# Performance work log

Hardware: AMD Instinct MI355X
Metric: run time of the kernel (lower is better)

The kernel has to match this reference:

```python
import jax, jax.numpy as jnp
import numpy as np

B, K, N = 8, 4, 131072
T = B * K * N  # upper bound on packed length
NEG_IDLE = -1e8   # logit value forced when slot is idle
NEG_FILL = -1000.0  # padded-output fill value for logits


def setup_inputs() -> dict:
    key = jax.random.key(0)
    k1, k2, k3, k4, k5, k6 = jax.random.split(key, 6)
    return {
        "rgb": jax.random.normal(k1, (T, 3), dtype=jnp.float32),
        "logits_surface": jax.random.normal(k2, (T, 1), dtype=jnp.float32),
        "logits_air": jax.random.normal(k3, (T, 1), dtype=jnp.float32),
        "mask_surface": jax.random.bernoulli(k4, 0.5, (B, K, N)),
        "mask_air": jax.random.bernoulli(k5, 0.5, (B, K, N)),
        "idle_states": jax.random.uniform(k6, (B, K), dtype=jnp.float32),
    }


def reference(rgb, logits_surface, logits_air, mask_surface, mask_air, idle_states):
    # Packed arrays are laid out in flattened (b, k, n) order: the packed index of a
    # masked element equals the count of True entries preceding it -> cumsum - 1.
    Bb, Kk, Nn = mask_surface.shape
    scale = (1.0 - idle_states)[:, :, None, None]          # [B,K,1,1]
    idle = idle_states[:, :, None, None]                   # [B,K,1,1]

    ms_flat = mask_surface.reshape(-1)
    idx_s = (jnp.cumsum(ms_flat.astype(jnp.int32)) - 1).reshape(Bb, Kk, Nn)
    ms = mask_surface[..., None]                           # [B,K,N,1]

    rgb_g = jnp.take(rgb, idx_s, axis=0)                   # [B,K,N,3]
    rgb_out = jnp.where(ms, rgb_g * scale, 0.0)

    ls_g = jnp.take(logits_surface, idx_s, axis=0)         # [B,K,N,1]
    logits_surface_out = jnp.where(ms, ls_g * scale + idle * NEG_IDLE, NEG_FILL)

    ma_flat = mask_air.reshape(-1)
    idx_a = (jnp.cumsum(ma_flat.astype(jnp.int32)) - 1).reshape(Bb, Kk, Nn)
    ma = mask_air[..., None]
    la_g = jnp.take(logits_air, idx_a, axis=0)             # [B,K,N,1]
    logits_air_out = jnp.where(ma, la_g * scale + idle * NEG_IDLE, NEG_FILL)

    return rgb_out, logits_surface_out, logits_air_out
```

## Files before the change

kernel.cpp:

```cpp
#include <hip/hip_runtime.h>
#include <stdint.h>

#define T_TOTAL  4194304
#define NEG_IDLE (-100000000.0f)
#define NEG_FILL (-1000.0f)

#define BLOCK   256
#define EPT     8
#define EPB     (BLOCK * EPT)
#define NBLOCKS (T_TOTAL / EPB)


typedef unsigned int u32x4 __attribute__((ext_vector_type(4)));

__device__ __forceinline__ unsigned decode8_i32(const u32x4 a, const u32x4 b) {
    return (a.x ? 1u : 0u) | (a.y ? 2u : 0u) | (a.z ? 4u : 0u) | (a.w ? 8u : 0u)
         | (b.x ? 16u : 0u) | (b.y ? 32u : 0u) | (b.z ? 64u : 0u) | (b.w ? 128u : 0u);
}

__global__ __launch_bounds__(BLOCK) void reduce_pack_kernel(
    const u32x4* __restrict__ ms,
    const u32x4* __restrict__ ma,
    unsigned long long* __restrict__ sums,
    unsigned short* __restrict__ packed)
{
    const int blk  = blockIdx.x;
    const int tid  = threadIdx.x;
    const int lane = tid & 63;
    const int wave = tid >> 6;
    const size_t e = (size_t)blk * EPB + (size_t)tid * EPT;

    const u32x4* ps = ms + (e >> 2);
    const u32x4* pa = ma + (e >> 2);
    const u32x4 s0 = __builtin_nontemporal_load(ps);
    const u32x4 s1 = __builtin_nontemporal_load(ps + 1);
    const u32x4 a0 = __builtin_nontemporal_load(pa);
    const u32x4 a1 = __builtin_nontemporal_load(pa + 1);
    const unsigned bits_s = decode8_i32(s0, s1);
    const unsigned bits_a = decode8_i32(a0, a1);
    packed[blk * BLOCK + tid] = (unsigned short)(bits_s | (bits_a << 8));

    unsigned long long v =
        ((unsigned long long)(unsigned)__popc(bits_a) << 32) | (unsigned)__popc(bits_s);
    #pragma unroll
    for (int d = 32; d; d >>= 1) v += __shfl_down(v, d, 64);

    __shared__ unsigned long long w[BLOCK / 64];
    if (lane == 0) w[wave] = v;
    __syncthreads();
    if (tid == 0) sums[blk] = w[0] + w[1] + w[2] + w[3];
}

__global__ __launch_bounds__(BLOCK) void scatter_kernel(
    const float* __restrict__ rgb,
    const float* __restrict__ ls,
    const float* __restrict__ la,
    const unsigned long long* __restrict__ sums,
    const unsigned short* __restrict__ packed,
    const float* __restrict__ idle_states,
    float* __restrict__ out)
{
    const int blk  = blockIdx.x;
    const int tid  = threadIdx.x;
    const int lane = tid & 63;
    const int wave = tid >> 6;
    const size_t base = (size_t)blk * EPB + (size_t)tid * EPT;

    const unsigned p = packed[blk * BLOCK + tid];
    const unsigned bits_s = p & 0xffu;
    const unsigned bits_a = p >> 8;

    unsigned long long acc = 0;
    {
        const ulonglong2* s2 = (const ulonglong2*)sums;
        const int i0 = lane * 32;
        #pragma unroll
        for (int q = 0; q < 16; ++q) {
            const ulonglong2 v = s2[lane * 16 + q];
            const int i = i0 + 2 * q;
            acc += (i     < blk) ? v.x : 0ull;
            acc += (i + 1 < blk) ? v.y : 0ull;
        }
    }
    #pragma unroll
    for (int w = 0; w < BLOCK / 64 - 1; ++w) {
        if (w < wave) {
            const unsigned pp = packed[blk * BLOCK + w * 64 + lane];
            acc += ((unsigned long long)(unsigned)__popc(pp >> 8) << 32)
                 | (unsigned)__popc(pp & 0xffu);
        }
    }
    #pragma unroll
    for (int d = 32; d; d >>= 1) acc += __shfl_xor(acc, d, 64);

    const unsigned long long pk =
        ((unsigned long long)(unsigned)__popc(bits_a) << 32) | (unsigned)__popc(bits_s);
    unsigned long long incl = pk;
    #pragma unroll
    for (int d = 1; d < 64; d <<= 1) {
        unsigned long long t = __shfl_up(incl, d, 64);
        if (lane >= d) incl += t;
    }
    const unsigned long long start = acc + (incl - pk);

    const int idx_s0 = (int)(start & 0xffffffffULL);
    const int idx_a0 = (int)(start >> 32);

    int is_[EPT], ia_[EPT];
    #pragma unroll
    for (int j = 0; j < EPT; ++j) {
        is_[j] = idx_s0 + __popc(bits_s & ((1u << j) - 1u));
        ia_[j] = idx_a0 + __popc(bits_a & ((1u << j) - 1u));
    }

    float r[3 * EPT], sv[EPT], av[EPT];
    #pragma unroll
    for (int j = 0; j < EPT; ++j) {
        const float* rp = rgb + (size_t)is_[j] * 3;
        r[3 * j + 0] = rp[0];
        r[3 * j + 1] = rp[1];
        r[3 * j + 2] = rp[2];
        sv[j] = ls[is_[j]];
        av[j] = la[ia_[j]];
    }

    const float idle      = idle_states[blk >> 6];
    const float scale     = 1.0f - idle;
    const float idle_term = idle * NEG_IDLE;
    #pragma unroll
    for (int j = 0; j < EPT; ++j) {
        const bool bs = (bits_s >> j) & 1u;
        const bool ba = (bits_a >> j) & 1u;
        r[3 * j + 0] = bs ? r[3 * j + 0] * scale : 0.0f;
        r[3 * j + 1] = bs ? r[3 * j + 1] * scale : 0.0f;
        r[3 * j + 2] = bs ? r[3 * j + 2] * scale : 0.0f;
        sv[j] = bs ? (sv[j] * scale + idle_term) : NEG_FILL;
        av[j] = ba ? (av[j] * scale + idle_term) : NEG_FILL;
    }

    float4* prgb = (float4*)(out + base * 3);
    #pragma unroll
    for (int j = 0; j < 6; ++j) prgb[j] = ((const float4*)r)[j];

    float4* pls = (float4*)(out + (size_t)3 * T_TOTAL + base);
    pls[0] = ((const float4*)sv)[0];
    pls[1] = ((const float4*)sv)[1];

    float4* pla = (float4*)(out + (size_t)4 * T_TOTAL + base);
    pla[0] = ((const float4*)av)[0];
    pla[1] = ((const float4*)av)[1];
}

extern "C" void kernel_launch(void* const* d_in, const int* in_sizes, int n_in,
                              void* d_out, int out_size, void* d_ws, size_t ws_size,
                              hipStream_t stream) {
    const float* rgb  = (const float*)d_in[0];
    const float* ls   = (const float*)d_in[1];
    const float* la   = (const float*)d_in[2];
    const u32x4* ms   = (const u32x4*)d_in[3];
    const u32x4* ma   = (const u32x4*)d_in[4];
    const float* idle = (const float*)d_in[5];
    float* out = (float*)d_out;

    unsigned long long* sums   = (unsigned long long*)d_ws;
    unsigned short*     packed = (unsigned short*)((uint8_t*)d_ws + NBLOCKS * sizeof(unsigned long long));

    reduce_pack_kernel<<<NBLOCKS, BLOCK, 0, stream>>>(ms, ma, sums, packed);
    scatter_kernel<<<NBLOCKS, BLOCK, 0, stream>>>(rgb, ls, la, sums, packed,
                                                  idle, out);
}
```

Measured before the change: 204.4 us.

## Stage surface gathers through LDS with coalesced block loads and swizzled stores

Each block now loads its contiguous range of packed rgb and surface logits into shared memory with coalesced loads, then gathers from LDS instead of doing scattered global loads. The rgb output is transposed through LDS so stores are coalesced float4 nontemporal writes. The prefix over block sums is spread across all 256 threads, and intra-block wave offsets now come from a shared-memory exchange instead of re-reading packed data. This adds extra syncthreads and about 34KB of LDS per block, which may reduce occupancy.

```diff
diff --git a/kernel.cpp b/kernel.cpp
--- a/kernel.cpp
+++ b/kernel.cpp
@@ -10,12 +10,18 @@
 #define EPB     (BLOCK * EPT)
 #define NBLOCKS (T_TOTAL / EPB)
 
+#define SWZ(d) ((d) + ((d) >> 5))
 
 typedef unsigned int u32x4 __attribute__((ext_vector_type(4)));
+typedef float        f32x4 __attribute__((ext_vector_type(4)));
 
 __device__ __forceinline__ unsigned decode8_i32(const u32x4 a, const u32x4 b) {
     return (a.x ? 1u : 0u) | (a.y ? 2u : 0u) | (a.z ? 4u : 0u) | (a.w ? 8u : 0u)
          | (b.x ? 16u : 0u) | (b.y ? 32u : 0u) | (b.z ? 64u : 0u) | (b.w ? 128u : 0u);
+}
+
+__device__ __forceinline__ f32x4 mk4(float a, float b, float c, float d) {
+    f32x4 v; v.x = a; v.y = b; v.z = c; v.w = d; return v;
 }
 
 __global__ __launch_bounds__(BLOCK) void reduce_pack_kernel(
@@ -60,38 +66,35 @@
     const float* __restrict__ idle_states,
     float* __restrict__ out)
 {
+    __shared__ float rgbb[6340];
+    __shared__ float lsb[2120];
+    __shared__ unsigned long long wtot[BLOCK / 64];
+    __shared__ unsigned long long wpre[BLOCK / 64];
+
     const int blk  = blockIdx.x;
     const int tid  = threadIdx.x;
     const int lane = tid & 63;
     const int wave = tid >> 6;
-    const size_t base = (size_t)blk * EPB + (size_t)tid * EPT;
 
     const unsigned p = packed[blk * BLOCK + tid];
     const unsigned bits_s = p & 0xffu;
     const unsigned bits_a = p >> 8;
+    const int cnt_s = (int)(unsigned)(sums[blk] & 0xffffffffu);
 
     unsigned long long acc = 0;
     {
         const ulonglong2* s2 = (const ulonglong2*)sums;
-        const int i0 = lane * 32;
+        const int i0 = tid * 8;
         #pragma unroll
-        for (int q = 0; q < 16; ++q) {
-            const ulonglong2 v = s2[lane * 16 + q];
+        for (int q = 0; q < 4; ++q) {
+            const ulonglong2 v = s2[tid * 4 + q];
             const int i = i0 + 2 * q;
             acc += (i     < blk) ? v.x : 0ull;
             acc += (i + 1 < blk) ? v.y : 0ull;
         }
-    }
-    #pragma unroll
-    for (int w = 0; w < BLOCK / 64 - 1; ++w) {
-        if (w < wave) {
-            const unsigned pp = packed[blk * BLOCK + w * 64 + lane];
-            acc += ((unsigned long long)(unsigned)__popc(pp >> 8) << 32)
-                 | (unsigned)__popc(pp & 0xffu);
-        }
-    }
-    #pragma unroll
-    for (int d = 32; d; d >>= 1) acc += __shfl_xor(acc, d, 64);
+        #pragma unroll
+        for (int d = 32; d; d >>= 1) acc += __shfl_down(acc, d, 64);
+    }
 
     const unsigned long long pk =
         ((unsigned long long)(unsigned)__popc(bits_a) << 32) | (unsigned)__popc(bits_s);
@@ -101,28 +104,68 @@
         unsigned long long t = __shfl_up(incl, d, 64);
         if (lane >= d) incl += t;
     }
-    const unsigned long long start = acc + (incl - pk);
-
-    const int idx_s0 = (int)(start & 0xffffffffULL);
-    const int idx_a0 = (int)(start >> 32);
-
-    int is_[EPT], ia_[EPT];
+    unsigned long long excl = incl - pk;
+
+    if (lane == 63) wtot[wave] = incl;
+    if (lane == 0)  wpre[wave] = acc;
+    __syncthreads();
+    #pragma unroll
+    for (int w = 0; w < BLOCK / 64; ++w)
+        if (w < wave) excl += wtot[w];
+    const unsigned long long pre = wpre[0] + wpre[1] + wpre[2] + wpre[3];
+    const unsigned long long st  = pre + excl;
+
+    const int start_s = (int)(unsigned)(pre & 0xffffffffu);
+    const int idx_a0  = (int)(st >> 32);
+    const int loc_s0  = (int)(unsigned)(st & 0xffffffffu) - start_s;
+
+    int ls_[EPT], ia_[EPT];
     #pragma unroll
     for (int j = 0; j < EPT; ++j) {
-        is_[j] = idx_s0 + __popc(bits_s & ((1u << j) - 1u));
+        ls_[j] = loc_s0 + __popc(bits_s & ((1u << j) - 1u));
         ia_[j] = idx_a0 + __popc(bits_a & ((1u << j) - 1u));
     }
 
-    float r[3 * EPT], sv[EPT], av[EPT];
+    float av[EPT];
+    #pragma unroll
+    for (int j = 0; j < EPT; ++j) av[j] = la[ia_[j]];
+
+    const float* rgb_g = rgb + (size_t)start_s * 3;
+    const float* ls_g  = ls + start_s;
+    const int c3 = cnt_s * 3;
+    float t24[24], t8[8];
+    #pragma unroll
+    for (int q = 0; q < 24; ++q) {
+        const int d = tid + 256 * q;
+        t24[q] = (d < c3) ? __builtin_nontemporal_load(rgb_g + d) : 0.0f;
+    }
+    #pragma unroll
+    for (int q = 0; q < 8; ++q) {
+        const int d = tid + 256 * q;
+        t8[q] = (d < cnt_s) ? __builtin_nontemporal_load(ls_g + d) : 0.0f;
+    }
+    #pragma unroll
+    for (int q = 0; q < 24; ++q) {
+        const int d = tid + 256 * q;
+        if (d < c3) rgbb[SWZ(d)] = t24[q];
+    }
+    #pragma unroll
+    for (int q = 0; q < 8; ++q) {
+        const int d = tid + 256 * q;
+        if (d < cnt_s) lsb[SWZ(d)] = t8[q];
+    }
+    __syncthreads();
+
+    float r[3 * EPT], sv[EPT];
     #pragma unroll
     for (int j = 0; j < EPT; ++j) {
-        const float* rp = rgb + (size_t)is_[j] * 3;
-        r[3 * j + 0] = rp[0];
-        r[3 * j + 1] = rp[1];
-        r[3 * j + 2] = rp[2];
-        sv[j] = ls[is_[j]];
-        av[j] = la[ia_[j]];
-    }
+        const int b = ls_[j] * 3;
+        r[3 * j + 0] = rgbb[SWZ(b)];
+        r[3 * j + 1] = rgbb[SWZ(b + 1)];
+        r[3 * j + 2] = rgbb[SWZ(b + 2)];
+        sv[j] = lsb[SWZ(ls_[j])];
+    }
+    __syncthreads();
 
     const float idle      = idle_states[blk >> 6];
     const float scale     = 1.0f - idle;
@@ -138,17 +181,30 @@
         av[j] = ba ? (av[j] * scale + idle_term) : NEG_FILL;
     }
 
-    float4* prgb = (float4*)(out + base * 3);
-    #pragma unroll
-    for (int j = 0; j < 6; ++j) prgb[j] = ((const float4*)r)[j];
-
-    float4* pls = (float4*)(out + (size_t)3 * T_TOTAL + base);
-    pls[0] = ((const float4*)sv)[0];
-    pls[1] = ((const float4*)sv)[1];
-
-    float4* pla = (float4*)(out + (size_t)4 * T_TOTAL + base);
-    pla[0] = ((const float4*)av)[0];
-    pla[1] = ((const float4*)av)[1];
+    const size_t base = (size_t)blk * EPB + (size_t)tid * EPT;
+    {
+        f32x4* pls = (f32x4*)(out + (size_t)3 * T_TOTAL + base);
+        __builtin_nontemporal_store(mk4(sv[0], sv[1], sv[2], sv[3]), pls);
+        __builtin_nontemporal_store(mk4(sv[4], sv[5], sv[6], sv[7]), pls + 1);
+        f32x4* pla = (f32x4*)(out + (size_t)4 * T_TOTAL + base);
+        __builtin_nontemporal_store(mk4(av[0], av[1], av[2], av[3]), pla);
+        __builtin_nontemporal_store(mk4(av[4], av[5], av[6], av[7]), pla + 1);
+    }
+
+    #pragma unroll
+    for (int j = 0; j < 3 * EPT; ++j) {
+        const int e = tid * 24 + j;
+        rgbb[SWZ(e)] = r[j];
+    }
+    __syncthreads();
+    float* out_rgb = out + (size_t)blk * (EPB * 3);
+    #pragma unroll
+    for (int i = 0; i < 6; ++i) {
+        const int g = tid * 4 + 1024 * i;
+        const f32x4 v = mk4(rgbb[SWZ(g)], rgbb[SWZ(g + 1)],
+                            rgbb[SWZ(g + 2)], rgbb[SWZ(g + 3)]);
+        __builtin_nontemporal_store(v, (f32x4*)(out_rgb + g));
+    }
 }
 
 extern "C" void kernel_launch(void* const* d_in, const int* in_sizes, int n_in,
```

After: 173.0 us. 15.4% less time.
